# Performance work log

Hardware: AMD Instinct MI355X
Metric: run time of the kernel (lower is better)

## Reference

```python
import jax, jax.numpy as jnp
import numpy as np

L = 12      # gpt2-small layers
D = 768     # n_embd
H = 12      # heads
NTOK = 60   # A5 group size / vocab
DST = 128   # d_state
B, T = 8, 1024
ID_ID = 0
INJECT = 8  # inject_layer


def _ln(x, g, b):
    m = x.mean(-1, keepdims=True)
    v = x.var(-1, keepdims=True)
    return (x - m) * jax.lax.rsqrt(v + 1e-5) * g + b


def _forward(tok_emb, state_emb, sp_w, sp_b, wh_w, wh_b, ws_w, ws_b, wd_w, wd_b,
             head_w, head_b, wpe, ln1_g, ln1_b, attn_w, attn_b, proj_w, proj_b,
             ln2_g, ln2_b, fc_w, fc_b, mproj_w, mproj_b, lnf_g, lnf_b,
             input_ids, mul):
    Bc, Tc = input_ids.shape
    # --- sequential group-recurrence state scan: s_{t+1} = mul[x_t, s_t] ---
    def step(s, ids_t):
        s2 = mul[ids_t, s]
        return s2, s2
    s0 = jnp.full((Bc,), ID_ID, jnp.int32)
    _, post = jax.lax.scan(step, s0, input_ids.T)   # [T, B] post-states
    post = post.T                                    # [B, T]
    pre = jnp.concatenate([jnp.full((Bc, 1), ID_ID, jnp.int32), post[:, :-1]], axis=1)
    # clean mode: inject PRE-states everywhere (mask == 1)
    s = state_emb[pre] @ sp_w + sp_b                 # [B, T, D] projected state channel
    # input_add injection
    x = tok_emb[input_ids] + s
    # --- frozen GPT-2 forward ---
    h = x + wpe[:Tc]
    hd = D // H
    scale = 1.0 / np.sqrt(hd)
    causal = jnp.tril(jnp.ones((Tc, Tc), bool))
    for l in range(L):
        a = _ln(h, ln1_g[l], ln1_b[l])
        qkv = a @ attn_w[l] + attn_b[l]
        q, k, v = jnp.split(qkv, 3, axis=-1)
        q = q.reshape(Bc, Tc, H, hd)
        k = k.reshape(Bc, Tc, H, hd)
        v = v.reshape(Bc, Tc, H, hd)
        sc = jnp.einsum('bthd,bshd->bhts', q, k) * scale
        sc = jnp.where(causal, sc, jnp.float32(-1e9))
        att = jax.nn.softmax(sc, axis=-1)
        o = jnp.einsum('bhts,bshd->bthd', att, v).reshape(Bc, Tc, D)
        h = h + o @ proj_w[l] + proj_b[l]
        m = _ln(h, ln2_g[l], ln2_b[l])
        h = h + jax.nn.gelu(m @ fc_w[l] + fc_b[l], approximate=True) @ mproj_w[l] + mproj_b[l]
        if l == INJECT:
            # gated residual fusion hook on block output
            gate = jax.nn.sigmoid(h @ wh_w + wh_b + s @ ws_w + ws_b)
            h = h + gate * (s @ wd_w + wd_b)
    h = _ln(h, lnf_g, lnf_b)
    logits = h[:, -1] @ head_w + head_b             # [B, NTOK]
    return logits


def setup_inputs() -> dict:
    key = jax.random.key(0)
    ks = iter(jax.random.split(key, 48))
    p = lambda *sh: (0.02 * jax.random.normal(next(ks), sh)).astype(jnp.float32)
    return dict(
        input_ids=jax.random.randint(next(ks), (B, T), 0, NTOK, jnp.int32),
        mul=jax.random.randint(next(ks), (NTOK, NTOK), 0, NTOK, jnp.int32),
        tok_emb=p(NTOK, D), state_emb=p(NTOK, DST),
        sp_w=p(DST, D), sp_b=jnp.zeros((D,), jnp.float32),
        wh_w=p(D, D), wh_b=jnp.zeros((D,), jnp.float32),
        ws_w=p(D, D), ws_b=jnp.zeros((D,), jnp.float32),
        wd_w=p(D, D), wd_b=jnp.zeros((D,), jnp.float32),
        head_w=p(D, NTOK), head_b=jnp.zeros((NTOK,), jnp.float32),
        wpe=p(T, D),
        ln1_g=jnp.ones((L, D), jnp.float32), ln1_b=jnp.zeros((L, D), jnp.float32),
        attn_w=p(L, D, 3 * D), attn_b=jnp.zeros((L, 3 * D), jnp.float32),
        proj_w=p(L, D, D), proj_b=jnp.zeros((L, D), jnp.float32),
        ln2_g=jnp.ones((L, D), jnp.float32), ln2_b=jnp.zeros((L, D), jnp.float32),
        fc_w=p(L, D, 4 * D), fc_b=jnp.zeros((L, 4 * D), jnp.float32),
        mproj_w=p(L, 4 * D, D), mproj_b=jnp.zeros((L, D), jnp.float32),
        lnf_g=jnp.ones((D,), jnp.float32), lnf_b=jnp.zeros((D,), jnp.float32),
    )


def reference(input_ids, mul, tok_emb, state_emb, sp_w, sp_b, wh_w, wh_b, ws_w, ws_b,
              wd_w, wd_b, head_w, head_b, wpe, ln1_g, ln1_b, attn_w, attn_b,
              proj_w, proj_b, ln2_g, ln2_b, fc_w, fc_b, mproj_w, mproj_b, lnf_g, lnf_b):
    return _forward(tok_emb, state_emb, sp_w, sp_b, wh_w, wh_b, ws_w, ws_b, wd_w, wd_b,
                    head_w, head_b, wpe, ln1_g, ln1_b, attn_w, attn_b, proj_w, proj_b,
                    ln2_g, ln2_b, fc_w, fc_b, mproj_w, mproj_b, lnf_g, lnf_b,
                    input_ids, mul)
```

## Files before the change

kernel.cpp:

```cpp
#include <hip/hip_runtime.h>
#include <hip/hip_bf16.h>
#include <math.h>

#define L_LAYERS 12
#define D_MODEL 768
#define H_HEADS 12
#define HD 64
#define NTOK 60
#define DST 128
#define BATCH 8
#define SEQ 1024
#define NT (BATCH * SEQ)
#define INJECT_L 8

typedef short bf16x8 __attribute__((ext_vector_type(8)));
typedef float f32x4 __attribute__((ext_vector_type(4)));
typedef unsigned short u16x4 __attribute__((ext_vector_type(4)));

__device__ __forceinline__ unsigned short f2bf(float f) {
    unsigned int u = __float_as_uint(f);
    u = (u + 0x7FFF + ((u >> 16) & 1)) >> 16;
    return (unsigned short)u;
}

__device__ __forceinline__ float gelu_fast(float x) {
    float two_c = 1.5957691216057308f * (x + 0.044715f * x * x * x);
    return x / (1.0f + __expf(-two_c));
}

__device__ __forceinline__ void async_copy16(void* lds, const void* gmem) {
    __builtin_amdgcn_global_load_lds(
        (const __attribute__((address_space(1))) unsigned int*)gmem,
        (__attribute__((address_space(3))) unsigned int*)lds,
        16, 0, 0);
}

__global__ __launch_bounds__(1024) void scan_kernel(const int* __restrict__ ids,
                                                    const int* __restrict__ mul,
                                                    int* __restrict__ pre) {
    __shared__ int smul[NTOK * NTOK];
    __shared__ int sids[SEQ];
    __shared__ int Mc[64 * NTOK];
    __shared__ int entry[64];
    int b = blockIdx.x;
    int tid = threadIdx.x;
    for (int i = tid; i < NTOK * NTOK; i += 1024) smul[i] = mul[i];
    for (int i = tid; i < SEQ; i += 1024) sids[i] = ids[b * SEQ + i];
    __syncthreads();
    for (int task = tid; task < 64 * NTOK; task += 1024) {
        int c = task / NTOK, s = task - c * NTOK;
        int st = s;
        #pragma unroll
        for (int j = 0; j < 16; j++) st = smul[sids[c * 16 + j] * NTOK + st];
        Mc[c * NTOK + s] = st;
    }
    __syncthreads();
    if (tid == 0) {
        int st = 0;
        for (int c = 0; c < 64; c++) { entry[c] = st; st = Mc[c * NTOK + st]; }
    }
    __syncthreads();
    if (tid < 64) {
        int c = tid;
        int st = entry[c];
        int* pr = pre + b * SEQ + c * 16;
        #pragma unroll
        for (int j = 0; j < 16; j++) {
            pr[j] = st;
            st = smul[sids[c * 16 + j] * NTOK + st];
        }
    }
}

__global__ __launch_bounds__(256) void state_table_kernel(const float* __restrict__ state_emb,
                                                          const float* __restrict__ sp_w,
                                                          const float* __restrict__ sp_b,
                                                          float* __restrict__ stable) {
    int st = blockIdx.x;
    __shared__ float se[DST];
    if (threadIdx.x < DST) se[threadIdx.x] = state_emb[st * DST + threadIdx.x];
    __syncthreads();
    for (int d = threadIdx.x; d < D_MODEL; d += 256) {
        float acc = sp_b[d];
        #pragma unroll 8
        for (int k = 0; k < DST; k++) acc += se[k] * sp_w[k * D_MODEL + d];
        stable[st * D_MODEL + d] = acc;
    }
}

__global__ __launch_bounds__(64) void embed_gather(const int* __restrict__ ids,
                                                   const int* __restrict__ pre,
                                                   const float* __restrict__ tok_emb,
                                                   const float* __restrict__ stable,
                                                   const float* __restrict__ wpe,
                                                   unsigned short* __restrict__ s_bf,
                                                   float* __restrict__ h) {
    int n = blockIdx.x;
    int t = n & (SEQ - 1);
    int lane = threadIdx.x;
    const float4* te = (const float4*)(tok_emb + (size_t)ids[n] * D_MODEL);
    const float4* sv = (const float4*)(stable + (size_t)pre[n] * D_MODEL);
    const float4* wp = (const float4*)(wpe + (size_t)t * D_MODEL);
    float4* hr = (float4*)(h + (size_t)n * D_MODEL);
    unsigned short* sr = s_bf + (size_t)n * D_MODEL;
    #pragma unroll
    for (int j = 0; j < 3; j++) {
        int idx = j * 64 + lane;
        float4 a = te[idx], b = sv[idx], c = wp[idx];
        float4 o;
        o.x = a.x + b.x + c.x; o.y = a.y + b.y + c.y;
        o.z = a.z + b.z + c.z; o.w = a.w + b.w + c.w;
        hr[idx] = o;
        u16x4 pk = { f2bf(b.x), f2bf(b.y), f2bf(b.z), f2bf(b.w) };
        *(u16x4*)&sr[idx * 4] = pk;
    }
}

__global__ __launch_bounds__(256) void ln_bf16_kernel(const float* __restrict__ x,
                                                      const float* __restrict__ g,
                                                      const float* __restrict__ bta,
                                                      unsigned short* __restrict__ out) {
    int row = blockIdx.x * 4 + (threadIdx.x >> 6);
    int lane = threadIdx.x & 63;
    const float4* xr = (const float4*)(x + (size_t)row * D_MODEL);
    float4 v[3];
    float sum = 0.f, sq = 0.f;
    #pragma unroll
    for (int j = 0; j < 3; j++) {
        v[j] = xr[j * 64 + lane];
        sum += v[j].x + v[j].y + v[j].z + v[j].w;
        sq += v[j].x * v[j].x + v[j].y * v[j].y + v[j].z * v[j].z + v[j].w * v[j].w;
    }
    for (int off = 32; off; off >>= 1) {
        sum += __shfl_xor(sum, off);
        sq += __shfl_xor(sq, off);
    }
    float mean = sum * (1.0f / D_MODEL);
    float var = sq * (1.0f / D_MODEL) - mean * mean;
    float r = rsqrtf(var + 1e-5f);
    const float4* g4 = (const float4*)g;
    const float4* b4 = (const float4*)bta;
    unsigned short* orow = out + (size_t)row * D_MODEL;
    #pragma unroll
    for (int j = 0; j < 3; j++) {
        int idx = j * 64 + lane;
        float4 gg = g4[idx], bb = b4[idx];
        u16x4 pk = { f2bf((v[j].x - mean) * r * gg.x + bb.x),
                     f2bf((v[j].y - mean) * r * gg.y + bb.y),
                     f2bf((v[j].z - mean) * r * gg.z + bb.z),
                     f2bf((v[j].w - mean) * r * gg.w + bb.w) };
        *(u16x4*)&orow[idx * 4] = pk;
    }
}

__global__ __launch_bounds__(256) void ln_f32_kernel(const float* __restrict__ x,
                                                     const float* __restrict__ g,
                                                     const float* __restrict__ bta,
                                                     float* __restrict__ out,
                                                     long in_stride, long out_stride) {
    long row = blockIdx.x;
    const float* xr = x + row * in_stride;
    int tid = threadIdx.x;
    float v0 = xr[tid], v1 = xr[tid + 256], v2 = xr[tid + 512];
    float sum = v0 + v1 + v2;
    float sq = v0 * v0 + v1 * v1 + v2 * v2;
    for (int off = 32; off; off >>= 1) {
        sum += __shfl_xor(sum, off);
        sq += __shfl_xor(sq, off);
    }
    __shared__ float red[8];
    int wid = tid >> 6;
    if ((tid & 63) == 0) { red[wid] = sum; red[4 + wid] = sq; }
    __syncthreads();
    sum = red[0] + red[1] + red[2] + red[3];
    sq = red[4] + red[5] + red[6] + red[7];
    float mean = sum * (1.0f / D_MODEL);
    float var = sq * (1.0f / D_MODEL) - mean * mean;
    float r = rsqrtf(var + 1e-5f);
    float* orow = out + row * out_stride;
    orow[tid] = (v0 - mean) * r * g[tid] + bta[tid];
    orow[tid + 256] = (v1 - mean) * r * g[tid + 256] + bta[tid + 256];
    orow[tid + 512] = (v2 - mean) * r * g[tid + 512] + bta[tid + 512];
}

__device__ __forceinline__ void conv_tile(const float* __restrict__ src,
                                          unsigned short* __restrict__ dst,
                                          int R, int C, int rt, int ct,
                                          int tc, int tr) {
    __shared__ float tile[32][33];
    int r0 = rt * 32, c0 = ct * 32;
    #pragma unroll
    for (int i = 0; i < 32; i += 8)
        tile[tr + i][tc] = src[(size_t)(r0 + tr + i) * C + c0 + tc];
    __syncthreads();
    #pragma unroll
    for (int i = 0; i < 32; i += 8)
        dst[(size_t)(c0 + tr + i) * R + r0 + tc] = f2bf(tile[tc][tr + i]);
}

__global__ __launch_bounds__(256) void wconv_layer(const float* __restrict__ attn_w,
                                                   const float* __restrict__ proj_w,
                                                   const float* __restrict__ fc_w,
                                                   const float* __restrict__ mproj_w,
                                                   unsigned short* __restrict__ attn_wt,
                                                   unsigned short* __restrict__ proj_wt,
                                                   unsigned short* __restrict__ fc_wt,
                                                   unsigned short* __restrict__ mproj_wt) {
    int bid = blockIdx.x;
    const float* src; unsigned short* dst; int R, C, CT, tloc;
    if (bid < 1728)      { src = attn_w;  dst = attn_wt;  R = 768;  C = 2304; CT = 72; tloc = bid; }
    else if (bid < 2304) { src = proj_w;  dst = proj_wt;  R = 768;  C = 768;  CT = 24; tloc = bid - 1728; }
    else if (bid < 4608) { src = fc_w;    dst = fc_wt;    R = 768;  C = 3072; CT = 96; tloc = bid - 2304; }
    else                 { src = mproj_w; dst = mproj_wt; R = 3072; C = 768;  CT = 24; tloc = bid - 4608; }
    int rt = tloc / CT, ct = tloc - rt * CT;
    conv_tile(src, dst, R, C, rt, ct, threadIdx.x, threadIdx.y);
}

__global__ __launch_bounds__(256) void wconv_inject(const float* __restrict__ wh_w,
                                                    const float* __restrict__ ws_w,
                                                    const float* __restrict__ wd_w,
                                                    unsigned short* __restrict__ wh_t,
                                                    unsigned short* __restrict__ ws_t,
                                                    unsigned short* __restrict__ wd_t) {
    int bid = blockIdx.x;
    int sel = bid / 576, tloc = bid - sel * 576;
    const float* src = sel == 0 ? wh_w : (sel == 1 ? ws_w : wd_w);
    unsigned short* dst = sel == 0 ? wh_t : (sel == 1 ? ws_t : wd_t);
    int rt = tloc / 24, ct = tloc - rt * 24;
    conv_tile(src, dst, 768, 768, rt, ct, threadIdx.x, threadIdx.y);
}

#define FLAG_OUTBF16 1
#define FLAG_GELU 2
#define FLAG_RESID 4
#define FLAG_MIRROR 8

__global__ __launch_bounds__(256) void mfma_gemm(const unsigned short* __restrict__ A,
                                                 const unsigned short* __restrict__ Wt,
                                                 const float* __restrict__ bias,
                                                 const float* __restrict__ residual,
                                                 float* __restrict__ Cf,
                                                 unsigned short* __restrict__ Cb,
                                                 unsigned short* __restrict__ Cmir,
                                                 int M, int K, int N, int flags) {
    __shared__ unsigned short As[128 * 64];
    __shared__ unsigned short Bs[128 * 64];
    int tid = threadIdx.x;
    int wave = tid >> 6, lane = tid & 63;
    int quad = lane >> 4, l16 = lane & 15;
    int m0 = blockIdx.x * 128, n0 = blockIdx.y * 128;
    int wm = (wave & 1) * 64, wn = (wave >> 1) * 64;
    f32x4 acc[4][4] = {};

    for (int k0 = 0; k0 < K; k0 += 64) {
        #pragma unroll
        for (int i = 0; i < 4; i++) {
            int chunk = i * 256 + wave * 64 + lane;
            int r = chunk >> 3;
            int cc = (chunk & 7) ^ (r & 7);
            async_copy16(&As[(i * 256 + wave * 64) * 8],
                         A + (size_t)(m0 + r) * K + k0 + cc * 8);
            async_copy16(&Bs[(i * 256 + wave * 64) * 8],
                         Wt + (size_t)(n0 + r) * K + k0 + cc * 8);
        }
        __syncthreads();
        #pragma unroll
        for (int sub = 0; sub < 2; sub++) {
            bf16x8 af[4], bfr[4];
            #pragma unroll
            for (int mi = 0; mi < 4; mi++) {
                int R = wm + mi * 16 + l16;
                int slot = (sub * 4 + quad) ^ (R & 7);
                af[mi] = *(const bf16x8*)&As[R * 64 + slot * 8];
            }
            #pragma unroll
            for (int ni = 0; ni < 4; ni++) {
                int R = wn + ni * 16 + l16;
                int slot = (sub * 4 + quad) ^ (R & 7);
                bfr[ni] = *(const bf16x8*)&Bs[R * 64 + slot * 8];
            }
            #pragma unroll
            for (int mi = 0; mi < 4; mi++)
                #pragma unroll
                for (int ni = 0; ni < 4; ni++)
                    acc[mi][ni] = __builtin_amdgcn_mfma_f32_16x16x32_bf16(
                        af[mi], bfr[ni], acc[mi][ni], 0, 0, 0);
        }
        __syncthreads();
    }
    #pragma unroll
    for (int mi = 0; mi < 4; mi++) {
        #pragma unroll
        for (int ni = 0; ni < 4; ni++) {
            int col = n0 + wn + ni * 16 + l16;
            float bv = bias[col];
            #pragma unroll
            for (int r = 0; r < 4; r++) {
                int row = m0 + wm + mi * 16 + quad * 4 + r;
                size_t idx = (size_t)row * N + col;
                float v = acc[mi][ni][r] + bv;
                if (flags & FLAG_RESID) v += residual[idx];
                if (flags & FLAG_GELU) v = gelu_fast(v);
                if (flags & FLAG_OUTBF16) Cb[idx] = f2bf(v);
                else Cf[idx] = v;
                if (flags & FLAG_MIRROR) Cmir[idx] = f2bf(v);
            }
        }
    }
}

__global__ __launch_bounds__(256) void attn_mfma(const unsigned short* __restrict__ qkv,
                                                 unsigned short* __restrict__ o) {
    int qt = gridDim.x - 1 - blockIdx.x;
    int hh = blockIdx.y, b = blockIdx.z;
    int tid = threadIdx.x, wave = tid >> 6, lane = tid & 63;
    int quad = lane >> 4, l16 = lane & 15;
    __shared__ unsigned short Ks[64][72];
    __shared__ unsigned short Vt[64][72];
    __shared__ unsigned short Ps[4][16][72];
    const size_t rstride = 3 * D_MODEL;
    int q0 = qt * 64;

    int qrow = q0 + wave * 16 + l16;
    const unsigned short* qp = qkv + ((size_t)(b * SEQ + qrow)) * rstride + hh * HD;
    bf16x8 qf0 = *(const bf16x8*)(qp + quad * 8);
    bf16x8 qf1 = *(const bf16x8*)(qp + 32 + quad * 8);

    float l_r = 0.f;
    f32x4 oacc[4] = {};

    uint4 kreg[2], vreg[2];
    {
        size_t kbase = ((size_t)(b * SEQ)) * rstride + D_MODEL + hh * HD;
        size_t vbase = kbase + D_MODEL;
        #pragma unroll
        for (int i = 0; i < 2; i++) {
            int chunk = i * 256 + tid;
            int r = chunk >> 3, cc = chunk & 7;
            kreg[i] = *(const uint4*)(qkv + kbase + (size_t)r * rstride + cc * 8);
        }
        #pragma unroll
        for (int i = 0; i < 2; i++) {
            int dg = i * 4 + wave;
            vreg[i] = *(const uint4*)(qkv + vbase + (size_t)lane * rstride + dg * 8);
        }
    }

    for (int kt = 0; kt <= qt; kt++) {
        __syncthreads();
        #pragma unroll
        for (int i = 0; i < 2; i++) {
            int chunk = i * 256 + tid;
            int r = chunk >> 3, cc = chunk & 7;
            *(uint4*)&Ks[r][cc * 8] = kreg[i];
        }
        #pragma unroll
        for (int i = 0; i < 2; i++) {
            int dg = i * 4 + wave;
            uint4 vv = vreg[i];
            const unsigned short* vs = (const unsigned short*)&vv;
            #pragma unroll
            for (int j = 0; j < 8; j++) Vt[dg * 8 + j][lane] = vs[j];
        }
        __syncthreads();

        if (kt < qt) {
            size_t kbase = ((size_t)(b * SEQ + (kt + 1) * 64)) * rstride + D_MODEL + hh * HD;
            size_t vbase = kbase + D_MODEL;
            #pragma unroll
            for (int i = 0; i < 2; i++) {
                int chunk = i * 256 + tid;
                int r = chunk >> 3, cc = chunk & 7;
                kreg[i] = *(const uint4*)(qkv + kbase + (size_t)r * rstride + cc * 8);
            }
            #pragma unroll
            for (int i = 0; i < 2; i++) {
                int dg = i * 4 + wave;
                vreg[i] = *(const uint4*)(qkv + vbase + (size_t)lane * rstride + dg * 8);
            }
        }

        f32x4 sacc[4] = {};
        __builtin_amdgcn_s_setprio(1);
        #pragma unroll
        for (int ni = 0; ni < 4; ni++) {
            bf16x8 kf0 = *(const bf16x8*)&Ks[ni * 16 + l16][quad * 8];
            bf16x8 kf1 = *(const bf16x8*)&Ks[ni * 16 + l16][32 + quad * 8];
            sacc[ni] = __builtin_amdgcn_mfma_f32_16x16x32_bf16(kf0, qf0, sacc[ni], 0, 0, 0);
            sacc[ni] = __builtin_amdgcn_mfma_f32_16x16x32_bf16(kf1, qf1, sacc[ni], 0, 0, 0);
        }
        __builtin_amdgcn_s_setprio(0);

        bool diag = (kt == qt);
        const float scale = 0.125f;
        int qloc = wave * 16 + l16;
        float lsg[4];
        #pragma unroll
        for (int ni = 0; ni < 4; ni++) {
            #pragma unroll
            for (int r = 0; r < 4; r++) {
                float pp = __expf(sacc[ni][r] * scale);
                if (diag && (ni * 16 + quad * 4 + r > qloc)) pp = 0.f;
                sacc[ni][r] = pp;
            }
            lsg[ni] = (sacc[ni][0] + sacc[ni][1]) + (sacc[ni][2] + sacc[ni][3]);
        }
        float ls = (lsg[0] + lsg[1]) + (lsg[2] + lsg[3]);
        ls += __shfl_xor(ls, 16);
        ls += __shfl_xor(ls, 32);
        l_r += ls;

        #pragma unroll
        for (int ni = 0; ni < 4; ni++) {
            u16x4 pk = { f2bf(sacc[ni][0]), f2bf(sacc[ni][1]),
                         f2bf(sacc[ni][2]), f2bf(sacc[ni][3]) };
            *(u16x4*)&Ps[wave][l16][ni * 16 + quad * 4] = pk;
        }
        asm volatile("s_waitcnt lgkmcnt(0)" ::: "memory");

        bf16x8 pf0 = *(const bf16x8*)&Ps[wave][l16][quad * 8];
        bf16x8 pf1 = *(const bf16x8*)&Ps[wave][l16][32 + quad * 8];
        __builtin_amdgcn_s_setprio(1);
        #pragma unroll
        for (int ni = 0; ni < 4; ni++) {
            bf16x8 vf0 = *(const bf16x8*)&Vt[ni * 16 + l16][quad * 8];
            bf16x8 vf1 = *(const bf16x8*)&Vt[ni * 16 + l16][32 + quad * 8];
            oacc[ni] = __builtin_amdgcn_mfma_f32_16x16x32_bf16(pf0, vf0, oacc[ni], 0, 0, 0);
            oacc[ni] = __builtin_amdgcn_mfma_f32_16x16x32_bf16(pf1, vf1, oacc[ni], 0, 0, 0);
        }
        __builtin_amdgcn_s_setprio(0);
    }

    float lt[4];
    #pragma unroll
    for (int r = 0; r < 4; r++) lt[r] = 1.0f / __shfl(l_r, quad * 4 + r);
    #pragma unroll
    for (int ni = 0; ni < 4; ni++) {
        #pragma unroll
        for (int r = 0; r < 4; r++) {
            int row = q0 + wave * 16 + quad * 4 + r;
            o[((size_t)(b * SEQ + row)) * D_MODEL + hh * HD + ni * 16 + l16] =
                f2bf(oacc[ni][r] * lt[r]);
        }
    }
}

__global__ __launch_bounds__(256) void gate_kernel(float* __restrict__ h,
                                                   const float* __restrict__ z,
                                                   const float* __restrict__ dv,
                                                   size_t total) {
    size_t i = (size_t)blockIdx.x * blockDim.x + threadIdx.x;
    size_t stride = (size_t)gridDim.x * blockDim.x;
    for (; i < total; i += stride) {
        float g = 1.0f / (1.0f + __expf(-z[i]));
        h[i] += g * dv[i];
    }
}

__global__ __launch_bounds__(64) void head_kernel(const float* __restrict__ hn,
                                                  const float* __restrict__ head_w,
                                                  const float* __restrict__ head_b,
                                                  float* __restrict__ out) {
    int b = blockIdx.x;
    int n = threadIdx.x;
    if (n < NTOK) {
        float acc = head_b[n];
        const float* hr = hn + b * D_MODEL;
        for (int k = 0; k < D_MODEL; k++) acc += hr[k] * head_w[k * NTOK + n];
        out[b * NTOK + n] = acc;
    }
}

extern "C" void kernel_launch(void* const* d_in, const int* in_sizes, int n_in,
                              void* d_out, int out_size, void* d_ws, size_t ws_size,
                              hipStream_t stream) {
    (void)in_sizes; (void)n_in; (void)out_size; (void)ws_size;
    const int* input_ids = (const int*)d_in[0];
    const int* mul       = (const int*)d_in[1];
    const float* tok_emb = (const float*)d_in[2];
    const float* state_emb = (const float*)d_in[3];
    const float* sp_w = (const float*)d_in[4];
    const float* sp_b = (const float*)d_in[5];
    const float* wh_w = (const float*)d_in[6];
    const float* wh_b = (const float*)d_in[7];
    const float* ws_w = (const float*)d_in[8];
    const float* ws_b = (const float*)d_in[9];
    const float* wd_w = (const float*)d_in[10];
    const float* wd_b = (const float*)d_in[11];
    const float* head_w = (const float*)d_in[12];
    const float* head_b = (const float*)d_in[13];
    const float* wpe  = (const float*)d_in[14];
    const float* ln1_g = (const float*)d_in[15];
    const float* ln1_b = (const float*)d_in[16];
    const float* attn_w = (const float*)d_in[17];
    const float* attn_b = (const float*)d_in[18];
    const float* proj_w = (const float*)d_in[19];
    const float* proj_b = (const float*)d_in[20];
    const float* ln2_g = (const float*)d_in[21];
    const float* ln2_b = (const float*)d_in[22];
    const float* fc_w = (const float*)d_in[23];
    const float* fc_b = (const float*)d_in[24];
    const float* mproj_w = (const float*)d_in[25];
    const float* mproj_b = (const float*)d_in[26];
    const float* lnf_g = (const float*)d_in[27];
    const float* lnf_b = (const float*)d_in[28];
    float* out = (float*)d_out;

    size_t off = 0;
    auto alloc = [&](size_t bytes) {
        void* p = (char*)d_ws + off;
        off += (bytes + 255) & ~(size_t)255;
        return p;
    };
    int* pre = (int*)alloc((size_t)NT * 4);
    float* stable = (float*)alloc((size_t)NTOK * D_MODEL * 4);
    unsigned short* s_bf   = (unsigned short*)alloc((size_t)NT * D_MODEL * 2);
    float* h               = (float*)alloc((size_t)NT * D_MODEL * 4);
    unsigned short* a_bf   = (unsigned short*)alloc((size_t)NT * D_MODEL * 2);
    unsigned short* qkv_bf = (unsigned short*)alloc((size_t)NT * 3 * D_MODEL * 2);
    unsigned short* u_bf   = (unsigned short*)alloc((size_t)NT * 4 * D_MODEL * 2);
    unsigned short* h8_bf  = (unsigned short*)alloc((size_t)NT * D_MODEL * 2);
    float* z  = (float*)alloc((size_t)NT * D_MODEL * 4);
    float* dv = (float*)alloc((size_t)NT * D_MODEL * 4);
    float* hn = (float*)alloc((size_t)BATCH * D_MODEL * 4);
    unsigned short* attn_wt  = (unsigned short*)alloc((size_t)2304 * 768 * 2);
    unsigned short* proj_wt  = (unsigned short*)alloc((size_t)768 * 768 * 2);
    unsigned short* fc_wt    = (unsigned short*)alloc((size_t)3072 * 768 * 2);
    unsigned short* mproj_wt = (unsigned short*)alloc((size_t)768 * 3072 * 2);
    unsigned short* wh_t = (unsigned short*)alloc((size_t)768 * 768 * 2);
    unsigned short* ws_t = (unsigned short*)alloc((size_t)768 * 768 * 2);
    unsigned short* wd_t = (unsigned short*)alloc((size_t)768 * 768 * 2);

    scan_kernel<<<BATCH, 1024, 0, stream>>>(input_ids, mul, pre);
    state_table_kernel<<<NTOK, 256, 0, stream>>>(state_emb, sp_w, sp_b, stable);
    embed_gather<<<NT, 64, 0, stream>>>(input_ids, pre, tok_emb, stable, wpe, s_bf, h);
    wconv_inject<<<1728, dim3(32, 8), 0, stream>>>(wh_w, ws_w, wd_w, wh_t, ws_t, wd_t);

    for (int l = 0; l < L_LAYERS; l++) {
        wconv_layer<<<6912, dim3(32, 8), 0, stream>>>(
            attn_w + (size_t)l * 768 * 2304, proj_w + (size_t)l * 768 * 768,
            fc_w + (size_t)l * 768 * 3072, mproj_w + (size_t)l * 3072 * 768,
            attn_wt, proj_wt, fc_wt, mproj_wt);

        ln_bf16_kernel<<<NT / 4, 256, 0, stream>>>(h, ln1_g + l * D_MODEL,
                                                   ln1_b + l * D_MODEL, a_bf);
        mfma_gemm<<<dim3(NT / 128, 2304 / 128), 256, 0, stream>>>(
            a_bf, attn_wt, attn_b + (size_t)l * 2304, nullptr,
            nullptr, qkv_bf, nullptr, NT, 768, 2304, FLAG_OUTBF16);
        attn_mfma<<<dim3(SEQ / 64, H_HEADS, BATCH), 256, 0, stream>>>(qkv_bf, a_bf);
        mfma_gemm<<<dim3(NT / 128, 768 / 128), 256, 0, stream>>>(
            a_bf, proj_wt, proj_b + (size_t)l * 768, h,
            h, nullptr, nullptr, NT, 768, 768, FLAG_RESID);
        ln_bf16_kernel<<<NT / 4, 256, 0, stream>>>(h, ln2_g + l * D_MODEL,
                                                   ln2_b + l * D_MODEL, a_bf);
        mfma_gemm<<<dim3(NT / 128, 3072 / 128), 256, 0, stream>>>(
            a_bf, fc_wt, fc_b + (size_t)l * 3072, nullptr,
            nullptr, u_bf, nullptr, NT, 768, 3072, FLAG_OUTBF16 | FLAG_GELU);
        int mpflags = FLAG_RESID | (l == INJECT_L ? FLAG_MIRROR : 0);
        mfma_gemm<<<dim3(NT / 128, 768 / 128), 256, 0, stream>>>(
            u_bf, mproj_wt, mproj_b + (size_t)l * 768, h,
            h, nullptr, h8_bf, NT, 3072, 768, mpflags);

        if (l == INJECT_L) {
            mfma_gemm<<<dim3(NT / 128, 768 / 128), 256, 0, stream>>>(
                h8_bf, wh_t, wh_b, nullptr, z, nullptr, nullptr, NT, 768, 768, 0);
            mfma_gemm<<<dim3(NT / 128, 768 / 128), 256, 0, stream>>>(
                s_bf, ws_t, ws_b, z, z, nullptr, nullptr, NT, 768, 768, FLAG_RESID);
            mfma_gemm<<<dim3(NT / 128, 768 / 128), 256, 0, stream>>>(
                s_bf, wd_t, wd_b, nullptr, dv, nullptr, nullptr, NT, 768, 768, 0);
            gate_kernel<<<dim3(2048), 256, 0, stream>>>(h, z, dv, (size_t)NT * D_MODEL);
        }
    }

    ln_f32_kernel<<<BATCH, 256, 0, stream>>>(h + (size_t)(SEQ - 1) * D_MODEL,
                                             lnf_g, lnf_b, hn,
                                             (long)SEQ * D_MODEL, D_MODEL);
    head_kernel<<<BATCH, 64, 0, stream>>>(hn, head_w, head_b, out);
}
```

Measured before the change: 4.383 ms.

## Split-K the N=768 projection GEMMs with atomic accumulation into residual

The attention output projection and MLP down-projection GEMMs (N=768, only 384 tiles) now use split-K with 2 and 4 partitions. Each partition atomically adds its partial sum into the fp32 residual stream h, and only partition 0 adds the bias. This replaces the explicit residual read. The aim is to put more workgroups on the GPU for these narrow GEMMs, at the cost of fp32 atomic traffic and non-deterministic summation order. Because the bf16 mirror output is removed, the injection layer needs a separate bf16 cast kernel.

```diff
diff --git a/kernel.cpp b/kernel.cpp
--- a/kernel.cpp
+++ b/kernel.cpp
@@ -233,7 +233,7 @@
 #define FLAG_OUTBF16 1
 #define FLAG_GELU 2
 #define FLAG_RESID 4
-#define FLAG_MIRROR 8
+#define FLAG_ATOMIC 8
 
 __global__ __launch_bounds__(256) void mfma_gemm(const unsigned short* __restrict__ A,
                                                  const unsigned short* __restrict__ Wt,
@@ -241,18 +241,21 @@
                                                  const float* __restrict__ residual,
                                                  float* __restrict__ Cf,
                                                  unsigned short* __restrict__ Cb,
-                                                 unsigned short* __restrict__ Cmir,
-                                                 int M, int K, int N, int flags) {
+                                                 int M, int K, int N, int flags,
+                                                 int ksplit) {
     __shared__ unsigned short As[128 * 64];
     __shared__ unsigned short Bs[128 * 64];
     int tid = threadIdx.x;
     int wave = tid >> 6, lane = tid & 63;
     int quad = lane >> 4, l16 = lane & 15;
     int m0 = blockIdx.x * 128, n0 = blockIdx.y * 128;
+    int kz = blockIdx.z;
+    int kchunk = K / ksplit;
+    int kbeg = kz * kchunk, kend = kbeg + kchunk;
     int wm = (wave & 1) * 64, wn = (wave >> 1) * 64;
     f32x4 acc[4][4] = {};
 
-    for (int k0 = 0; k0 < K; k0 += 64) {
+    for (int k0 = kbeg; k0 < kend; k0 += 64) {
         #pragma unroll
         for (int i = 0; i < 4; i++) {
             int chunk = i * 256 + wave * 64 + lane;
@@ -293,19 +296,34 @@
         #pragma unroll
         for (int ni = 0; ni < 4; ni++) {
             int col = n0 + wn + ni * 16 + l16;
-            float bv = bias[col];
+            float bv = (kz == 0) ? bias[col] : 0.f;
             #pragma unroll
             for (int r = 0; r < 4; r++) {
                 int row = m0 + wm + mi * 16 + quad * 4 + r;
                 size_t idx = (size_t)row * N + col;
                 float v = acc[mi][ni][r] + bv;
-                if (flags & FLAG_RESID) v += residual[idx];
-                if (flags & FLAG_GELU) v = gelu_fast(v);
-                if (flags & FLAG_OUTBF16) Cb[idx] = f2bf(v);
-                else Cf[idx] = v;
-                if (flags & FLAG_MIRROR) Cmir[idx] = f2bf(v);
+                if (flags & FLAG_ATOMIC) {
+                    atomicAdd(&Cf[idx], v);
+                } else {
+                    if (flags & FLAG_RESID) v += residual[idx];
+                    if (flags & FLAG_GELU) v = gelu_fast(v);
+                    if (flags & FLAG_OUTBF16) Cb[idx] = f2bf(v);
+                    else Cf[idx] = v;
+                }
             }
         }
+    }
+}
+
+__global__ __launch_bounds__(256) void bf16cast_kernel(const float* __restrict__ in,
+                                                       unsigned short* __restrict__ out,
+                                                       size_t total4) {
+    size_t i = (size_t)blockIdx.x * blockDim.x + threadIdx.x;
+    size_t stride = (size_t)gridDim.x * blockDim.x;
+    for (; i < total4; i += stride) {
+        float4 v = ((const float4*)in)[i];
+        u16x4 pk = { f2bf(v.x), f2bf(v.y), f2bf(v.z), f2bf(v.w) };
+        *(u16x4*)&out[i * 4] = pk;
     }
 }
 
@@ -546,28 +564,29 @@
                                                    ln1_b + l * D_MODEL, a_bf);
         mfma_gemm<<<dim3(NT / 128, 2304 / 128), 256, 0, stream>>>(
             a_bf, attn_wt, attn_b + (size_t)l * 2304, nullptr,
-            nullptr, qkv_bf, nullptr, NT, 768, 2304, FLAG_OUTBF16);
+            nullptr, qkv_bf, NT, 768, 2304, FLAG_OUTBF16, 1);
         attn_mfma<<<dim3(SEQ / 64, H_HEADS, BATCH), 256, 0, stream>>>(qkv_bf, a_bf);
-        mfma_gemm<<<dim3(NT / 128, 768 / 128), 256, 0, stream>>>(
-            a_bf, proj_wt, proj_b + (size_t)l * 768, h,
-            h, nullptr, nullptr, NT, 768, 768, FLAG_RESID);
+        mfma_gemm<<<dim3(NT / 128, 768 / 128, 2), 256, 0, stream>>>(
+            a_bf, proj_wt, proj_b + (size_t)l * 768, nullptr,
+            h, nullptr, NT, 768, 768, FLAG_ATOMIC, 2);
         ln_bf16_kernel<<<NT / 4, 256, 0, stream>>>(h, ln2_g + l * D_MODEL,
                                                    ln2_b + l * D_MODEL, a_bf);
         mfma_gemm<<<dim3(NT / 128, 3072 / 128), 256, 0, stream>>>(
             a_bf, fc_wt, fc_b + (size_t)l * 3072, nullptr,
-            nullptr, u_bf, nullptr, NT, 768, 3072, FLAG_OUTBF16 | FLAG_GELU);
-        int mpflags = FLAG_RESID | (l == INJECT_L ? FLAG_MIRROR : 0);
-        mfma_gemm<<<dim3(NT / 128, 768 / 128), 256, 0, stream>>>(
-            u_bf, mproj_wt, mproj_b + (size_t)l * 768, h,
-            h, nullptr, h8_bf, NT, 3072, 768, mpflags);
+            nullptr, u_bf, NT, 768, 3072, FLAG_OUTBF16 | FLAG_GELU, 1);
+        mfma_gemm<<<dim3(NT / 128, 768 / 128, 4), 256, 0, stream>>>(
+            u_bf, mproj_wt, mproj_b + (size_t)l * 768, nullptr,
+            h, nullptr, NT, 3072, 768, FLAG_ATOMIC, 4);
 
         if (l == INJECT_L) {
+            bf16cast_kernel<<<dim3(2048), 256, 0, stream>>>(
+                h, h8_bf, (size_t)NT * D_MODEL / 4);
             mfma_gemm<<<dim3(NT / 128, 768 / 128), 256, 0, stream>>>(
-                h8_bf, wh_t, wh_b, nullptr, z, nullptr, nullptr, NT, 768, 768, 0);
+                h8_bf, wh_t, wh_b, nullptr, z, nullptr, NT, 768, 768, 0, 1);
             mfma_gemm<<<dim3(NT / 128, 768 / 128), 256, 0, stream>>>(
-                s_bf, ws_t, ws_b, z, z, nullptr, nullptr, NT, 768, 768, FLAG_RESID);
+                s_bf, ws_t, ws_b, z, z, nullptr, NT, 768, 768, FLAG_RESID, 1);
             mfma_gemm<<<dim3(NT / 128, 768 / 128), 256, 0, stream>>>(
-                s_bf, wd_t, wd_b, nullptr, dv, nullptr, nullptr, NT, 768, 768, 0);
+                s_bf, wd_t, wd_b, nullptr, dv, nullptr, NT, 768, 768, 0, 1);
             gate_kernel<<<dim3(2048), 256, 0, stream>>>(h, z, dv, (size_t)NT * D_MODEL);
         }
     }
```

After: 4.950 ms. +12.9%, slower.
